# Kernel optimization log

Hardware: AMD Instinct MI355X
Metric: run time of the kernel (lower is better)

Reference implementation:

```python
import jax, jax.numpy as jnp
import numpy as np

EMBED = 1024
HEADS = 16
HEAD_DIM = EMBED // HEADS
BATCH = 4
SEQ = 2048


def setup_inputs() -> dict:
    key = jax.random.key(0)
    ks = jax.random.split(key, 9)
    s = 1.0 / np.sqrt(EMBED)
    inp = {
        "x": jax.random.normal(ks[0], (BATCH, SEQ, EMBED), dtype=jnp.float32),
        "Wq": jax.random.normal(ks[1], (EMBED, EMBED), dtype=jnp.float32) * s,
        "bq": jnp.zeros((EMBED,), jnp.float32),
        "Wk": jax.random.normal(ks[2], (EMBED, EMBED), dtype=jnp.float32) * s,
        "bk": jnp.zeros((EMBED,), jnp.float32),
        "Wv": jax.random.normal(ks[3], (EMBED, EMBED), dtype=jnp.float32) * s,
        "bv": jnp.zeros((EMBED,), jnp.float32),
        "Wo": jax.random.normal(ks[4], (EMBED, EMBED), dtype=jnp.float32) * s,
        "bo": jnp.zeros((EMBED,), jnp.float32),
    }
    return inp


def reference(x, Wq, bq, Wk, bk, Wv, bv, Wo, bo):
    B, S, E = x.shape
    H, D = HEADS, HEAD_DIM
    # projections (torch Linear with weight stored as [in,out] here)
    q = (x @ Wq + bq).reshape(B, S, H, D).transpose(0, 2, 1, 3)  # [B,H,S,D]
    k = (x @ Wk + bk).reshape(B, S, H, D).transpose(0, 2, 1, 3)
    v = (x @ Wv + bv).reshape(B, S, H, D).transpose(0, 2, 1, 3)
    scores = jnp.einsum('bhqd,bhkd->bhqk', q, k) * (1.0 / np.sqrt(D))
    causal = jnp.tril(jnp.ones((S, S), dtype=bool))
    scores = jnp.where(causal[None, None], scores, -jnp.inf)
    attn = jax.nn.softmax(scores, axis=-1)  # dropout p=0.0 -> identity
    out = jnp.einsum('bhqk,bhkd->bhqd', attn, v)  # [B,H,S,D]
    out = out.transpose(0, 2, 1, 3).reshape(B, S, E)
    return out @ Wo + bo
```

## Files before the change

kernel.cpp:

```cpp
#include <hip/hip_runtime.h>
#include <stdint.h>

#define EMBED 1024
#define SEQ   2048
#define BATCH 4
#define HEADS 16
#define HDIM  64
#define LDP   72

typedef unsigned short ushort_t;
typedef __bf16 bf16x8 __attribute__((ext_vector_type(8)));
typedef ushort_t u16x8 __attribute__((ext_vector_type(8)));
typedef float  f32x4  __attribute__((ext_vector_type(4)));

#define MFMA16 __builtin_amdgcn_mfma_f32_16x16x32_bf16

typedef __attribute__((address_space(3))) uint32_t lds_u32_t;
typedef __attribute__((address_space(1))) const uint32_t glb_u32_t;

__device__ __forceinline__ void gl_lds16(const ushort_t* g, ushort_t* l) {
    __builtin_amdgcn_global_load_lds((glb_u32_t*)g, (lds_u32_t*)l, 16, 0, 0);
}

__device__ __forceinline__ ushort_t f2bf(float f) {
    union { float f; uint32_t u; } c; c.f = f;
    uint32_t u = c.u;
    return (ushort_t)((u + 0x7FFFu + ((u >> 16) & 1u)) >> 16);
}

__global__ __launch_bounds__(256)
void cast_x(const float* __restrict__ X, ushort_t* __restrict__ Xb)
{
    size_t i = ((size_t)blockIdx.x * 256 + threadIdx.x) * 8;
    ushort_t tmp[8];
    #pragma unroll
    for (int e = 0; e < 8; ++e) tmp[e] = f2bf(X[i + e]);
    *(uint4*)(Xb + i) = *(const uint4*)tmp;
}

__global__ __launch_bounds__(256)
void cast_transpose_w(const float* __restrict__ W, ushort_t* __restrict__ Wt)
{
    __shared__ ushort_t Ts[64 * 80];
    const int t = threadIdx.x;
    const int k0 = blockIdx.x * 64, n0 = blockIdx.y * 64;
    const int r = t >> 2, cs = (t & 3) * 16;
    const float* src = W + (size_t)(k0 + r) * EMBED + n0 + cs;
    #pragma unroll
    for (int e = 0; e < 16; ++e) Ts[(cs + e) * 80 + r] = f2bf(src[e]);
    __syncthreads();
    const int n = t >> 2, ks = (t & 3) * 16;
    ushort_t* dst = Wt + (size_t)(n0 + n) * EMBED + k0 + ks;
    *(uint4*)(dst)     = *(const uint4*)(&Ts[n * 80 + ks]);
    *(uint4*)(dst + 8) = *(const uint4*)(&Ts[n * 80 + ks + 8]);
}

__global__ __launch_bounds__(256)
void gemm_qkv(const ushort_t* __restrict__ A, const ushort_t* __restrict__ Bt,
              const float* __restrict__ bq, const float* __restrict__ bk,
              const float* __restrict__ bv, ushort_t* __restrict__ Cq, size_t tsz)
{
    __shared__ ushort_t As[128 * 32];
    __shared__ ushort_t Bs[128 * 32];
    const int t = threadIdx.x;
    const int wave = t >> 6, lane = t & 63;
    const int l15 = lane & 15, quad = lane >> 4;
    const int m0 = blockIdx.y * 128, n0 = blockIdx.x * 128;
    const int wm = (wave >> 1) * 64, wn = (wave & 1) * 64;
    f32x4 acc[4][4] = {};

    const int srow = wave * 32 + (lane >> 2), scol = (lane & 3) * 8;
    const ushort_t* Ag = A  + (size_t)(m0 + srow) * EMBED + scol;
    const ushort_t* Bg = Bt + (size_t)(n0 + srow) * EMBED + scol;
    ushort_t* AsW = As + wave * 1024;
    ushort_t* BsW = Bs + wave * 1024;

    for (int k0 = 0; k0 < EMBED; k0 += 32) {
        gl_lds16(Ag + k0,              AsW);
        gl_lds16(Ag + k0 + 16 * EMBED, AsW + 512);
        gl_lds16(Bg + k0,              BsW);
        gl_lds16(Bg + k0 + 16 * EMBED, BsW + 512);
        __syncthreads();

        bf16x8 af[4], bfr[4];
        #pragma unroll
        for (int mt = 0; mt < 4; ++mt)
            af[mt] = *(const bf16x8*)(&As[(wm + mt * 16 + l15) * 32 + quad * 8]);
        #pragma unroll
        for (int nt = 0; nt < 4; ++nt)
            bfr[nt] = *(const bf16x8*)(&Bs[(wn + nt * 16 + l15) * 32 + quad * 8]);
        #pragma unroll
        for (int mt = 0; mt < 4; ++mt)
            #pragma unroll
            for (int nt = 0; nt < 4; ++nt)
                acc[mt][nt] = MFMA16(af[mt], bfr[nt], acc[mt][nt], 0, 0, 0);
        __syncthreads();
    }

    const int mat = blockIdx.x >> 3;
    const float* bias = (mat == 0) ? bq : (mat == 1) ? bk : bv;
    const float scale = (mat == 0) ? 0.125f : 1.0f;
    ushort_t* C = Cq + (size_t)mat * tsz;
    const int nc0 = (blockIdx.x & 7) * 128;
    #pragma unroll
    for (int nt = 0; nt < 4; ++nt) {
        int col = nc0 + wn + nt * 16 + l15;
        float bb = bias[col];
        #pragma unroll
        for (int mt = 0; mt < 4; ++mt)
            #pragma unroll
            for (int r = 0; r < 4; ++r) {
                int row = m0 + wm + mt * 16 + quad * 4 + r;
                C[(size_t)row * EMBED + col] = f2bf((acc[mt][nt][r] + bb) * scale);
            }
    }
}

__global__ __launch_bounds__(256)
void gemm_o(const ushort_t* __restrict__ A, const ushort_t* __restrict__ Bt,
            const float* __restrict__ bias, float* __restrict__ C)
{
    __shared__ ushort_t As[128 * 32];
    __shared__ ushort_t Bs[128 * 32];
    const int t = threadIdx.x;
    const int wave = t >> 6, lane = t & 63;
    const int l15 = lane & 15, quad = lane >> 4;
    const int m0 = blockIdx.y * 128, n0 = blockIdx.x * 128;
    const int wm = (wave >> 1) * 64, wn = (wave & 1) * 64;
    f32x4 acc[4][4] = {};

    const int srow = wave * 32 + (lane >> 2), scol = (lane & 3) * 8;
    const ushort_t* Ag = A  + (size_t)(m0 + srow) * EMBED + scol;
    const ushort_t* Bg = Bt + (size_t)(n0 + srow) * EMBED + scol;
    ushort_t* AsW = As + wave * 1024;
    ushort_t* BsW = Bs + wave * 1024;

    for (int k0 = 0; k0 < EMBED; k0 += 32) {
        gl_lds16(Ag + k0,              AsW);
        gl_lds16(Ag + k0 + 16 * EMBED, AsW + 512);
        gl_lds16(Bg + k0,              BsW);
        gl_lds16(Bg + k0 + 16 * EMBED, BsW + 512);
        __syncthreads();

        bf16x8 af[4], bfr[4];
        #pragma unroll
        for (int mt = 0; mt < 4; ++mt)
            af[mt] = *(const bf16x8*)(&As[(wm + mt * 16 + l15) * 32 + quad * 8]);
        #pragma unroll
        for (int nt = 0; nt < 4; ++nt)
            bfr[nt] = *(const bf16x8*)(&Bs[(wn + nt * 16 + l15) * 32 + quad * 8]);
        #pragma unroll
        for (int mt = 0; mt < 4; ++mt)
            #pragma unroll
            for (int nt = 0; nt < 4; ++nt)
                acc[mt][nt] = MFMA16(af[mt], bfr[nt], acc[mt][nt], 0, 0, 0);
        __syncthreads();
    }

    #pragma unroll
    for (int nt = 0; nt < 4; ++nt) {
        int col = n0 + wn + nt * 16 + l15;
        float bb = bias[col];
        #pragma unroll
        for (int mt = 0; mt < 4; ++mt)
            #pragma unroll
            for (int r = 0; r < 4; ++r) {
                int row = m0 + wm + mt * 16 + quad * 4 + r;
                C[(size_t)row * EMBED + col] = acc[mt][nt][r] + bb;
            }
    }
}

__global__ __launch_bounds__(256)
void transpose_v(const ushort_t* __restrict__ V, ushort_t* __restrict__ Vt)
{
    int blk = blockIdx.x;
    int st = blk & 31, bh = blk >> 5;
    int h = bh & 15, b = bh >> 4;
    int s0 = st * 64;
    __shared__ ushort_t Ts[64 * LDP];
    int tid = threadIdx.x;
    int r = tid >> 2, g = (tid & 3) * 8;

    const ushort_t* src = V + ((size_t)(b * SEQ + s0 + r)) * EMBED + h * HDIM;
    uint4 v0 = *(const uint4*)(src + g);
    uint4 v1 = *(const uint4*)(src + g + 32);
    const ushort_t* e0 = (const ushort_t*)&v0;
    const ushort_t* e1 = (const ushort_t*)&v1;
    #pragma unroll
    for (int e = 0; e < 8; ++e) Ts[(g + e) * LDP + r] = e0[e];
    #pragma unroll
    for (int e = 0; e < 8; ++e) Ts[(g + 32 + e) * LDP + r] = e1[e];
    __syncthreads();

    int d = tid >> 2;
    ushort_t* dst = Vt + ((size_t)bh * HDIM + d) * SEQ + s0;
    *(uint4*)(dst + g)      = *(const uint4*)(&Ts[d * LDP + g]);
    *(uint4*)(dst + g + 32) = *(const uint4*)(&Ts[d * LDP + g + 32]);
}

__global__ __launch_bounds__(256)
void flash_attn(const ushort_t* __restrict__ Q, const ushort_t* __restrict__ K,
                const ushort_t* __restrict__ Vt, ushort_t* __restrict__ O)
{
    const int blk = blockIdx.x;
    const int p = blk & 15, bh = blk >> 4;
    const int h = bh & 15, b = bh >> 4;
    const int t = threadIdx.x, wave = t >> 6, lane = t & 63;
    const int l15 = lane & 15, quad = lane >> 4;
    const int i0m[2] = { p * 64 + wave * 16, (31 - p) * 64 + wave * 16 };
    const int lastj[2] = { p, 31 - p };
    const size_t qkbase = (size_t)b * SEQ * EMBED + (size_t)h * HDIM;
    const size_t vtbase = (size_t)bh * HDIM * SEQ;

    __shared__ ushort_t Ks[64 * LDP];
    __shared__ ushort_t Vs[64 * LDP];
    __shared__ ushort_t Ps[4][32 * LDP];
    ushort_t* psw = &Ps[wave][0];

    bf16x8 qa[2][2];
    #pragma unroll
    for (int mt = 0; mt < 2; ++mt)
        #pragma unroll
        for (int ks = 0; ks < 2; ++ks)
            qa[mt][ks] = *(const bf16x8*)(Q + qkbase + (size_t)(i0m[mt] + l15) * EMBED + ks * 32 + quad * 8);

    union { uint32_t u[4]; bf16x8 v; } onesu;
    onesu.u[0] = onesu.u[1] = onesu.u[2] = onesu.u[3] = 0x3F803F80u;
    const bf16x8 ones = onesu.v;

    const int tr = t >> 2, tseg = (t & 3) * 16;
    const ushort_t* Kg = K  + qkbase + (size_t)tr * EMBED + tseg;
    const ushort_t* Vg = Vt + vtbase + (size_t)tr * SEQ + tseg;
    ushort_t* KsT = &Ks[tr * LDP + tseg];
    ushort_t* VsT = &Vs[tr * LDP + tseg];

    const int lastjb = 31 - p;
    uint4 ka0 = *(const uint4*)(Kg);
    uint4 ka1 = *(const uint4*)(Kg + 8);
    uint4 va0 = *(const uint4*)(Vg);
    uint4 va1 = *(const uint4*)(Vg + 8);

    f32x4 o_acc[2][4] = {};
    f32x4 l_acc[2] = {};

    for (int jt = 0; jt <= lastjb; ++jt) {
        *(uint4*)(KsT)     = ka0;
        *(uint4*)(KsT + 8) = ka1;
        *(uint4*)(VsT)     = va0;
        *(uint4*)(VsT + 8) = va1;
        if (jt < lastjb) {
            const ushort_t* Kn = Kg + (size_t)(jt + 1) * 64 * EMBED;
            const ushort_t* Vn = Vg + (size_t)(jt + 1) * 64;
            ka0 = *(const uint4*)(Kn);
            ka1 = *(const uint4*)(Kn + 8);
            va0 = *(const uint4*)(Vn);
            va1 = *(const uint4*)(Vn + 8);
        }
        __syncthreads();

        const int j0 = jt * 64;
        const bool act0 = (jt <= lastj[0]);

        f32x4 s[2][4] = {};
        #pragma unroll
        for (int ks = 0; ks < 2; ++ks)
            #pragma unroll
            for (int ct = 0; ct < 4; ++ct) {
                bf16x8 kb = *(const bf16x8*)(&Ks[(ct * 16 + l15) * LDP + ks * 32 + quad * 8]);
                if (act0) s[0][ct] = MFMA16(qa[0][ks], kb, s[0][ct], 0, 0, 0);
                s[1][ct] = MFMA16(qa[1][ks], kb, s[1][ct], 0, 0, 0);
            }

        #pragma unroll
        for (int mt = 0; mt < 2; ++mt) {
            if (mt == 0 && !act0) continue;
            if (jt == lastj[mt]) {
                #pragma unroll
                for (int ct = 0; ct < 4; ++ct)
                    #pragma unroll
                    for (int r = 0; r < 4; ++r) {
                        float pv = __expf(s[mt][ct][r]);
                        if (j0 + ct * 16 + l15 > i0m[mt] + quad * 4 + r) pv = 0.f;
                        union { float f; uint32_t u; } cv; cv.f = pv;
                        psw[(mt * 16 + quad * 4 + r) * LDP + ct * 16 + l15] = (ushort_t)(cv.u >> 16);
                    }
            } else {
                #pragma unroll
                for (int ct = 0; ct < 4; ++ct)
                    #pragma unroll
                    for (int r = 0; r < 4; ++r) {
                        float pv = __expf(s[mt][ct][r]);
                        union { float f; uint32_t u; } cv; cv.f = pv;
                        psw[(mt * 16 + quad * 4 + r) * LDP + ct * 16 + l15] = (ushort_t)(cv.u >> 16);
                    }
            }
        }

        #pragma unroll
        for (int mt = 0; mt < 2; ++mt) {
            if (mt == 0 && !act0) continue;
            #pragma unroll
            for (int ks = 0; ks < 2; ++ks) {
                union { u16x8 s; bf16x8 b; } pr;
                pr.s = *(const u16x8*)(&psw[(mt * 16 + l15) * LDP + ks * 32 + quad * 8]);
                bf16x8 pa = pr.b;
                l_acc[mt] = MFMA16(pa, ones, l_acc[mt], 0, 0, 0);
                #pragma unroll
                for (int dt = 0; dt < 4; ++dt) {
                    bf16x8 vb = *(const bf16x8*)(&Vs[(dt * 16 + l15) * LDP + ks * 32 + quad * 8]);
                    o_acc[mt][dt] = MFMA16(pa, vb, o_acc[mt][dt], 0, 0, 0);
                }
            }
        }
        __syncthreads();
    }

    #pragma unroll
    for (int mt = 0; mt < 2; ++mt)
        #pragma unroll
        for (int r = 0; r < 4; ++r) {
            float invl = 1.f / l_acc[mt][r];
            size_t ob = qkbase + (size_t)(i0m[mt] + quad * 4 + r) * EMBED;
            #pragma unroll
            for (int dt = 0; dt < 4; ++dt)
                O[ob + dt * 16 + l15] = f2bf(o_acc[mt][dt][r] * invl);
        }
}

extern "C" void kernel_launch(void* const* d_in, const int* in_sizes, int n_in,
                              void* d_out, int out_size, void* d_ws, size_t ws_size,
                              hipStream_t stream)
{
    (void)in_sizes; (void)n_in; (void)out_size; (void)ws_size;
    const float* x  = (const float*)d_in[0];
    const float* Wq = (const float*)d_in[1];
    const float* bq = (const float*)d_in[2];
    const float* Wk = (const float*)d_in[3];
    const float* bk = (const float*)d_in[4];
    const float* Wv = (const float*)d_in[5];
    const float* bv = (const float*)d_in[6];
    const float* Wo = (const float*)d_in[7];
    const float* bo = (const float*)d_in[8];
    float* out = (float*)d_out;

    const int M = BATCH * SEQ;
    size_t tsz = (size_t)M * EMBED;
    size_t wsz = (size_t)EMBED * EMBED;
    ushort_t* xb  = (ushort_t*)d_ws;
    ushort_t* Qb  = xb + tsz;
    ushort_t* Kb  = Qb + tsz;
    ushort_t* Vb  = Kb + tsz;
    ushort_t* Vt  = Vb + tsz;
    ushort_t* Wt0 = Vt + tsz;
    ushort_t* Wt1 = Wt0 + wsz;
    ushort_t* Wt2 = Wt1 + wsz;
    ushort_t* Wt3 = Wt2 + wsz;
    ushort_t* Ob  = xb;

    dim3 wg(16, 16);
    cast_x<<<4096, 256, 0, stream>>>(x, xb);
    cast_transpose_w<<<wg, 256, 0, stream>>>(Wq, Wt0);
    cast_transpose_w<<<wg, 256, 0, stream>>>(Wk, Wt1);
    cast_transpose_w<<<wg, 256, 0, stream>>>(Wv, Wt2);
    cast_transpose_w<<<wg, 256, 0, stream>>>(Wo, Wt3);

    gemm_qkv<<<dim3(24, 64), 256, 0, stream>>>(xb, Wt0, bq, bk, bv, Qb, tsz);

    transpose_v<<<BATCH * HEADS * (SEQ / 64), 256, 0, stream>>>(Vb, Vt);
    flash_attn<<<BATCH * HEADS * (SEQ / 128), 256, 0, stream>>>(Qb, Kb, Vt, Ob);

    gemm_o<<<dim3(8, 64), 256, 0, stream>>>(Ob, Wt3, bo, out);
}
```

Measured before the change: 294.3 us.

## Double-buffer GEMM and attention tiles via direct LDS loads, four query tiles per block

Both projection GEMMs now double-buffer their LDS tiles, prefetching the next K-slice with global_load_lds while MFMAs run on the current one. This leaves one barrier per iteration instead of two. The attention kernel also uses double-buffered direct-to-LDS loads for K and V and processes four balanced query tiles per block (p, 15-p, 16+p, 31-p), halving the grid. Each K/V tile is reused across more query rows, and the K/V fragments are hoisted out of the per-tile loop. It computes S transposed so P is written with packed 8-byte stores, at the cost of more registers per thread, with launch_bounds(256,2) asking for two blocks per SIMD.

```diff
diff --git a/kernel.cpp b/kernel.cpp
--- a/kernel.cpp
+++ b/kernel.cpp
@@ -27,6 +27,14 @@
     uint32_t u = c.u;
     return (ushort_t)((u + 0x7FFFu + ((u >> 16) & 1u)) >> 16);
 }
+__device__ __forceinline__ uint32_t bftrunc(float f) {
+    union { float f; uint32_t u; } c; c.f = f;
+    return c.u >> 16;
+}
+
+template <typename T> __device__ __forceinline__ void stf(T* p, size_t i, float v);
+template <> __device__ __forceinline__ void stf<float>(float* p, size_t i, float v) { p[i] = v; }
+template <> __device__ __forceinline__ void stf<ushort_t>(ushort_t* p, size_t i, float v) { p[i] = f2bf(v); }
 
 __global__ __launch_bounds__(256)
 void cast_x(const float* __restrict__ X, ushort_t* __restrict__ Xb)
@@ -60,8 +68,8 @@
               const float* __restrict__ bq, const float* __restrict__ bk,
               const float* __restrict__ bv, ushort_t* __restrict__ Cq, size_t tsz)
 {
-    __shared__ ushort_t As[128 * 32];
-    __shared__ ushort_t Bs[128 * 32];
+    __shared__ ushort_t As[2][128 * 32];
+    __shared__ ushort_t Bs[2][128 * 32];
     const int t = threadIdx.x;
     const int wave = t >> 6, lane = t & 63;
     const int l15 = lane & 15, quad = lane >> 4;
@@ -72,29 +80,35 @@
     const int srow = wave * 32 + (lane >> 2), scol = (lane & 3) * 8;
     const ushort_t* Ag = A  + (size_t)(m0 + srow) * EMBED + scol;
     const ushort_t* Bg = Bt + (size_t)(n0 + srow) * EMBED + scol;
-    ushort_t* AsW = As + wave * 1024;
-    ushort_t* BsW = Bs + wave * 1024;
-
-    for (int k0 = 0; k0 < EMBED; k0 += 32) {
-        gl_lds16(Ag + k0,              AsW);
-        gl_lds16(Ag + k0 + 16 * EMBED, AsW + 512);
-        gl_lds16(Bg + k0,              BsW);
-        gl_lds16(Bg + k0 + 16 * EMBED, BsW + 512);
+    const int wbase = wave * 1024;
+
+    gl_lds16(Ag,              &As[0][wbase]);
+    gl_lds16(Ag + 16 * EMBED, &As[0][wbase + 512]);
+    gl_lds16(Bg,              &Bs[0][wbase]);
+    gl_lds16(Bg + 16 * EMBED, &Bs[0][wbase + 512]);
+
+    for (int it = 0; it < 32; ++it) {
         __syncthreads();
-
+        const int cur = it & 1;
+        if (it < 31) {
+            const int nxt = cur ^ 1, k0 = (it + 1) * 32;
+            gl_lds16(Ag + k0,              &As[nxt][wbase]);
+            gl_lds16(Ag + k0 + 16 * EMBED, &As[nxt][wbase + 512]);
+            gl_lds16(Bg + k0,              &Bs[nxt][wbase]);
+            gl_lds16(Bg + k0 + 16 * EMBED, &Bs[nxt][wbase + 512]);
+        }
         bf16x8 af[4], bfr[4];
         #pragma unroll
         for (int mt = 0; mt < 4; ++mt)
-            af[mt] = *(const bf16x8*)(&As[(wm + mt * 16 + l15) * 32 + quad * 8]);
+            af[mt] = *(const bf16x8*)(&As[cur][(wm + mt * 16 + l15) * 32 + quad * 8]);
         #pragma unroll
         for (int nt = 0; nt < 4; ++nt)
-            bfr[nt] = *(const bf16x8*)(&Bs[(wn + nt * 16 + l15) * 32 + quad * 8]);
+            bfr[nt] = *(const bf16x8*)(&Bs[cur][(wn + nt * 16 + l15) * 32 + quad * 8]);
         #pragma unroll
         for (int mt = 0; mt < 4; ++mt)
             #pragma unroll
             for (int nt = 0; nt < 4; ++nt)
                 acc[mt][nt] = MFMA16(af[mt], bfr[nt], acc[mt][nt], 0, 0, 0);
-        __syncthreads();
     }
 
     const int mat = blockIdx.x >> 3;
@@ -120,8 +134,8 @@
 void gemm_o(const ushort_t* __restrict__ A, const ushort_t* __restrict__ Bt,
             const float* __restrict__ bias, float* __restrict__ C)
 {
-    __shared__ ushort_t As[128 * 32];
-    __shared__ ushort_t Bs[128 * 32];
+    __shared__ ushort_t As[2][128 * 32];
+    __shared__ ushort_t Bs[2][128 * 32];
     const int t = threadIdx.x;
     const int wave = t >> 6, lane = t & 63;
     const int l15 = lane & 15, quad = lane >> 4;
@@ -132,29 +146,35 @@
     const int srow = wave * 32 + (lane >> 2), scol = (lane & 3) * 8;
     const ushort_t* Ag = A  + (size_t)(m0 + srow) * EMBED + scol;
     const ushort_t* Bg = Bt + (size_t)(n0 + srow) * EMBED + scol;
-    ushort_t* AsW = As + wave * 1024;
-    ushort_t* BsW = Bs + wave * 1024;
-
-    for (int k0 = 0; k0 < EMBED; k0 += 32) {
-        gl_lds16(Ag + k0,              AsW);
-        gl_lds16(Ag + k0 + 16 * EMBED, AsW + 512);
-        gl_lds16(Bg + k0,              BsW);
-        gl_lds16(Bg + k0 + 16 * EMBED, BsW + 512);
+    const int wbase = wave * 1024;
+
+    gl_lds16(Ag,              &As[0][wbase]);
+    gl_lds16(Ag + 16 * EMBED, &As[0][wbase + 512]);
+    gl_lds16(Bg,              &Bs[0][wbase]);
+    gl_lds16(Bg + 16 * EMBED, &Bs[0][wbase + 512]);
+
+    for (int it = 0; it < 32; ++it) {
         __syncthreads();
-
+        const int cur = it & 1;
+        if (it < 31) {
+            const int nxt = cur ^ 1, k0 = (it + 1) * 32;
+            gl_lds16(Ag + k0,              &As[nxt][wbase]);
+            gl_lds16(Ag + k0 + 16 * EMBED, &As[nxt][wbase + 512]);
+            gl_lds16(Bg + k0,              &Bs[nxt][wbase]);
+            gl_lds16(Bg + k0 + 16 * EMBED, &Bs[nxt][wbase + 512]);
+        }
         bf16x8 af[4], bfr[4];
         #pragma unroll
         for (int mt = 0; mt < 4; ++mt)
-            af[mt] = *(const bf16x8*)(&As[(wm + mt * 16 + l15) * 32 + quad * 8]);
+            af[mt] = *(const bf16x8*)(&As[cur][(wm + mt * 16 + l15) * 32 + quad * 8]);
         #pragma unroll
         for (int nt = 0; nt < 4; ++nt)
-            bfr[nt] = *(const bf16x8*)(&Bs[(wn + nt * 16 + l15) * 32 + quad * 8]);
+            bfr[nt] = *(const bf16x8*)(&Bs[cur][(wn + nt * 16 + l15) * 32 + quad * 8]);
         #pragma unroll
         for (int mt = 0; mt < 4; ++mt)
             #pragma unroll
             for (int nt = 0; nt < 4; ++nt)
                 acc[mt][nt] = MFMA16(af[mt], bfr[nt], acc[mt][nt], 0, 0, 0);
-        __syncthreads();
     }
 
     #pragma unroll
@@ -199,129 +219,128 @@
     *(uint4*)(dst + g + 32) = *(const uint4*)(&Ts[d * LDP + g + 32]);
 }
 
-__global__ __launch_bounds__(256)
+__global__ __launch_bounds__(256, 2)
 void flash_attn(const ushort_t* __restrict__ Q, const ushort_t* __restrict__ K,
                 const ushort_t* __restrict__ Vt, ushort_t* __restrict__ O)
 {
     const int blk = blockIdx.x;
-    const int p = blk & 15, bh = blk >> 4;
+    const int p = blk & 7, bh = blk >> 3;
     const int h = bh & 15, b = bh >> 4;
     const int t = threadIdx.x, wave = t >> 6, lane = t & 63;
     const int l15 = lane & 15, quad = lane >> 4;
-    const int i0m[2] = { p * 64 + wave * 16, (31 - p) * 64 + wave * 16 };
-    const int lastj[2] = { p, 31 - p };
+    const int S[4] = { p, 15 - p, 16 + p, 31 - p };
+    int i0[4];
+    #pragma unroll
+    for (int mt = 0; mt < 4; ++mt) i0[mt] = S[mt] * 64 + wave * 16;
     const size_t qkbase = (size_t)b * SEQ * EMBED + (size_t)h * HDIM;
     const size_t vtbase = (size_t)bh * HDIM * SEQ;
 
-    __shared__ ushort_t Ks[64 * LDP];
-    __shared__ ushort_t Vs[64 * LDP];
-    __shared__ ushort_t Ps[4][32 * LDP];
+    __shared__ ushort_t Ks[2][64 * 64];
+    __shared__ ushort_t Vs[2][64 * 64];
+    __shared__ ushort_t Ps[4][64 * LDP];
     ushort_t* psw = &Ps[wave][0];
 
-    bf16x8 qa[2][2];
-    #pragma unroll
-    for (int mt = 0; mt < 2; ++mt)
+    bf16x8 qa[4][2];
+    #pragma unroll
+    for (int mt = 0; mt < 4; ++mt)
         #pragma unroll
         for (int ks = 0; ks < 2; ++ks)
-            qa[mt][ks] = *(const bf16x8*)(Q + qkbase + (size_t)(i0m[mt] + l15) * EMBED + ks * 32 + quad * 8);
+            qa[mt][ks] = *(const bf16x8*)(Q + qkbase + (size_t)(i0[mt] + l15) * EMBED + ks * 32 + quad * 8);
 
     union { uint32_t u[4]; bf16x8 v; } onesu;
     onesu.u[0] = onesu.u[1] = onesu.u[2] = onesu.u[3] = 0x3F803F80u;
     const bf16x8 ones = onesu.v;
 
-    const int tr = t >> 2, tseg = (t & 3) * 16;
-    const ushort_t* Kg = K  + qkbase + (size_t)tr * EMBED + tseg;
-    const ushort_t* Vg = Vt + vtbase + (size_t)tr * SEQ + tseg;
-    ushort_t* KsT = &Ks[tr * LDP + tseg];
-    ushort_t* VsT = &Vs[tr * LDP + tseg];
-
-    const int lastjb = 31 - p;
-    uint4 ka0 = *(const uint4*)(Kg);
-    uint4 ka1 = *(const uint4*)(Kg + 8);
-    uint4 va0 = *(const uint4*)(Vg);
-    uint4 va1 = *(const uint4*)(Vg + 8);
-
-    f32x4 o_acc[2][4] = {};
-    f32x4 l_acc[2] = {};
+    const int strow = wave * 16 + (lane >> 3);
+    const int stcol = (lane & 7) * 8;
+    const ushort_t* Kg = K  + qkbase + (size_t)strow * EMBED + stcol;
+    const ushort_t* Vg = Vt + vtbase + (size_t)strow * SEQ + stcol;
+    const int wb = wave * 1024;
+
+    const int lastjb = S[3];
+    gl_lds16(Kg,             &Ks[0][wb]);
+    gl_lds16(Kg + 8 * EMBED, &Ks[0][wb + 512]);
+    gl_lds16(Vg,             &Vs[0][wb]);
+    gl_lds16(Vg + 8 * SEQ,   &Vs[0][wb + 512]);
+
+    f32x4 o_acc[4][4] = {};
+    f32x4 l_acc[4] = {};
 
     for (int jt = 0; jt <= lastjb; ++jt) {
-        *(uint4*)(KsT)     = ka0;
-        *(uint4*)(KsT + 8) = ka1;
-        *(uint4*)(VsT)     = va0;
-        *(uint4*)(VsT + 8) = va1;
+        __syncthreads();
+        const int cur = jt & 1;
         if (jt < lastjb) {
-            const ushort_t* Kn = Kg + (size_t)(jt + 1) * 64 * EMBED;
-            const ushort_t* Vn = Vg + (size_t)(jt + 1) * 64;
-            ka0 = *(const uint4*)(Kn);
-            ka1 = *(const uint4*)(Kn + 8);
-            va0 = *(const uint4*)(Vn);
-            va1 = *(const uint4*)(Vn + 8);
-        }
-        __syncthreads();
-
+            const int nxt = cur ^ 1;
+            const size_t ko = (size_t)(jt + 1) * 64;
+            gl_lds16(Kg + ko * EMBED,             &Ks[nxt][wb]);
+            gl_lds16(Kg + ko * EMBED + 8 * EMBED, &Ks[nxt][wb + 512]);
+            gl_lds16(Vg + ko,                     &Vs[nxt][wb]);
+            gl_lds16(Vg + ko + 8 * SEQ,           &Vs[nxt][wb + 512]);
+        }
         const int j0 = jt * 64;
-        const bool act0 = (jt <= lastj[0]);
-
-        f32x4 s[2][4] = {};
+
+        bf16x8 kb[2][4];
         #pragma unroll
         for (int ks = 0; ks < 2; ++ks)
             #pragma unroll
-            for (int ct = 0; ct < 4; ++ct) {
-                bf16x8 kb = *(const bf16x8*)(&Ks[(ct * 16 + l15) * LDP + ks * 32 + quad * 8]);
-                if (act0) s[0][ct] = MFMA16(qa[0][ks], kb, s[0][ct], 0, 0, 0);
-                s[1][ct] = MFMA16(qa[1][ks], kb, s[1][ct], 0, 0, 0);
-            }
-
-        #pragma unroll
-        for (int mt = 0; mt < 2; ++mt) {
-            if (mt == 0 && !act0) continue;
-            if (jt == lastj[mt]) {
+            for (int ct = 0; ct < 4; ++ct)
+                kb[ks][ct] = *(const bf16x8*)(&Ks[cur][(ct * 16 + l15) * 64 + ks * 32 + quad * 8]);
+
+        #pragma unroll
+        for (int mt = 0; mt < 4; ++mt) {
+            if (jt > S[mt]) continue;
+            f32x4 s[4] = {};
+            #pragma unroll
+            for (int ks = 0; ks < 2; ++ks)
                 #pragma unroll
                 for (int ct = 0; ct < 4; ++ct)
-                    #pragma unroll
-                    for (int r = 0; r < 4; ++r) {
-                        float pv = __expf(s[mt][ct][r]);
-                        if (j0 + ct * 16 + l15 > i0m[mt] + quad * 4 + r) pv = 0.f;
-                        union { float f; uint32_t u; } cv; cv.f = pv;
-                        psw[(mt * 16 + quad * 4 + r) * LDP + ct * 16 + l15] = (ushort_t)(cv.u >> 16);
-                    }
-            } else {
-                #pragma unroll
-                for (int ct = 0; ct < 4; ++ct)
-                    #pragma unroll
-                    for (int r = 0; r < 4; ++r) {
-                        float pv = __expf(s[mt][ct][r]);
-                        union { float f; uint32_t u; } cv; cv.f = pv;
-                        psw[(mt * 16 + quad * 4 + r) * LDP + ct * 16 + l15] = (ushort_t)(cv.u >> 16);
-                    }
+                    s[ct] = MFMA16(kb[ks][ct], qa[mt][ks], s[ct], 0, 0, 0);
+            const bool dia = (jt == S[mt]);
+            const int qg = i0[mt] + l15;
+            #pragma unroll
+            for (int ct = 0; ct < 4; ++ct) {
+                float pv0 = __expf(s[ct][0]), pv1 = __expf(s[ct][1]);
+                float pv2 = __expf(s[ct][2]), pv3 = __expf(s[ct][3]);
+                if (dia) {
+                    int kg = j0 + ct * 16 + quad * 4;
+                    if (kg + 0 > qg) pv0 = 0.f;
+                    if (kg + 1 > qg) pv1 = 0.f;
+                    if (kg + 2 > qg) pv2 = 0.f;
+                    if (kg + 3 > qg) pv3 = 0.f;
+                }
+                uint32_t d0 = (bftrunc(pv1) << 16) | bftrunc(pv0);
+                uint32_t d1 = (bftrunc(pv3) << 16) | bftrunc(pv2);
+                uint2 w; w.x = d0; w.y = d1;
+                *(uint2*)(&psw[(mt * 16 + l15) * LDP + ct * 16 + quad * 4]) = w;
             }
         }
 
         #pragma unroll
-        for (int mt = 0; mt < 2; ++mt) {
-            if (mt == 0 && !act0) continue;
-            #pragma unroll
-            for (int ks = 0; ks < 2; ++ks) {
+        for (int ks = 0; ks < 2; ++ks) {
+            bf16x8 vb[4];
+            #pragma unroll
+            for (int dt = 0; dt < 4; ++dt)
+                vb[dt] = *(const bf16x8*)(&Vs[cur][(dt * 16 + l15) * 64 + ks * 32 + quad * 8]);
+            #pragma unroll
+            for (int mt = 0; mt < 4; ++mt) {
+                if (jt > S[mt]) continue;
                 union { u16x8 s; bf16x8 b; } pr;
                 pr.s = *(const u16x8*)(&psw[(mt * 16 + l15) * LDP + ks * 32 + quad * 8]);
                 bf16x8 pa = pr.b;
                 l_acc[mt] = MFMA16(pa, ones, l_acc[mt], 0, 0, 0);
                 #pragma unroll
-                for (int dt = 0; dt < 4; ++dt) {
-                    bf16x8 vb = *(const bf16x8*)(&Vs[(dt * 16 + l15) * LDP + ks * 32 + quad * 8]);
-                    o_acc[mt][dt] = MFMA16(pa, vb, o_acc[mt][dt], 0, 0, 0);
-                }
+                for (int dt = 0; dt < 4; ++dt)
+                    o_acc[mt][dt] = MFMA16(pa, vb[dt], o_acc[mt][dt], 0, 0, 0);
             }
         }
-        __syncthreads();
-    }
-
-    #pragma unroll
-    for (int mt = 0; mt < 2; ++mt)
+    }
+
+    #pragma unroll
+    for (int mt = 0; mt < 4; ++mt)
         #pragma unroll
         for (int r = 0; r < 4; ++r) {
             float invl = 1.f / l_acc[mt][r];
-            size_t ob = qkbase + (size_t)(i0m[mt] + quad * 4 + r) * EMBED;
+            size_t ob = qkbase + (size_t)(i0[mt] + quad * 4 + r) * EMBED;
             #pragma unroll
             for (int dt = 0; dt < 4; ++dt)
                 O[ob + dt * 16 + l15] = f2bf(o_acc[mt][dt][r] * invl);
@@ -368,7 +387,7 @@
     gemm_qkv<<<dim3(24, 64), 256, 0, stream>>>(xb, Wt0, bq, bk, bv, Qb, tsz);
 
     transpose_v<<<BATCH * HEADS * (SEQ / 64), 256, 0, stream>>>(Vb, Vt);
-    flash_attn<<<BATCH * HEADS * (SEQ / 128), 256, 0, stream>>>(Qb, Kb, Vt, Ob);
+    flash_attn<<<BATCH * HEADS * 8, 256, 0, stream>>>(Qb, Kb, Vt, Ob);
 
     gemm_o<<<dim3(8, 64), 256, 0, stream>>>(Ob, Wt3, bo, out);
 }
```

Result: no change. 295.8 us (+0.5%).
